# Kernel tuning notes

Hardware: AMD Instinct MI355X
Metric: run time of the kernel (lower is better)

Reference implementation:

```python
import jax, jax.numpy as jnp
import numpy as np

T, OBS, H, NOBJ = 32768, 256, 512, 4


def _xavier(key, shape):
    fan_in, fan_out = shape[0], shape[1]
    lim = jnp.sqrt(6.0 / (fan_in + fan_out)).astype(jnp.float32)
    return jax.random.uniform(key, shape, jnp.float32, -lim, lim)


def setup_inputs() -> dict:
    key = jax.random.key(0)
    ks = jax.random.split(key, 16)
    # weights stored as [in, out] so y = x @ W (same math as nn.Linear with W.T)
    return {
        "x": jax.random.normal(ks[0], (T, OBS), jnp.float32),
        "W_in0": _xavier(ks[1], (OBS, H)),
        "W_B0": _xavier(ks[2], (OBS, H)),
        "W_C0": _xavier(ks[3], (OBS, H)),
        "W_d0": _xavier(ks[4], (OBS, H)),
        "A_log0": jax.random.normal(ks[5], (H,), jnp.float32),
        "W_in1": _xavier(ks[6], (H, H)),
        "W_B1": _xavier(ks[7], (H, H)),
        "W_C1": _xavier(ks[8], (H, H)),
        "W_d1": _xavier(ks[9], (H, H)),
        "A_log1": jax.random.normal(ks[10], (H,), jnp.float32),
        "W_out": _xavier(ks[11], (H, NOBJ)),
        "b_out": jnp.zeros((NOBJ,), jnp.float32),
        "W_skip": _xavier(ks[12], (OBS, NOBJ)),
    }


def _mamba_layer(x, W_in, W_B, W_C, W_d, A_log):
    # x: [T, D_in] -> [T, H]
    x_state = x @ W_in           # [T, H]
    B = x @ W_B                  # [T, H]
    C = x @ W_C                  # [T, H]
    delta = jax.nn.sigmoid(x @ W_d)  # [T, H]
    A = -jnp.exp(A_log)          # [H]
    A_bar = jnp.exp(delta * A)   # [T, H], in (0, 1)
    Bx = B * x_state             # [T, H]

    def step(h, inp):
        a_t, bx_t = inp
        h = a_t * h + bx_t
        return h, h

    h0 = jnp.zeros((x_state.shape[-1],), x_state.dtype)
    _, h_seq = jax.lax.scan(step, h0, (A_bar, Bx))  # [T, H]
    return C * h_seq


def reference(x, W_in0, W_B0, W_C0, W_d0, A_log0,
              W_in1, W_B1, W_C1, W_d1, A_log1,
              W_out, b_out, W_skip):
    skip = x
    y = _mamba_layer(x, W_in0, W_B0, W_C0, W_d0, A_log0)
    y = _mamba_layer(y, W_in1, W_B1, W_C1, W_d1, A_log1)
    out = y @ W_out + b_out + skip @ W_skip  # [T, NOBJ]
    return out
```

## Files before the change

kernel.cpp:

```cpp
#include <hip/hip_runtime.h>

typedef __attribute__((ext_vector_type(8))) short short8;
typedef __attribute__((ext_vector_type(4))) float floatx4;

#define T_SIZE 32768
#define OBS    256
#define H      512
#define NC     1024
#define CHUNK  32
#define NGRP   64
#define GCH    16
#define SLAB   ((size_t)T_SIZE * 32)

__device__ __forceinline__ unsigned short f2bf(float f){
    union { float f; unsigned u; } v; v.f = f;
    unsigned u = v.u;
    u += 0x7FFFu + ((u >> 16) & 1u);
    return (unsigned short)(u >> 16);
}
__device__ __forceinline__ float bf2f(unsigned short u){
    union { unsigned u; float f; } v; v.u = ((unsigned)u) << 16; return v.f;
}

#define GLOAD_LDS16(g, l) \
    __builtin_amdgcn_global_load_lds((const __attribute__((address_space(1))) unsigned*)(g), \
                                     (__attribute__((address_space(3))) unsigned*)(l), 16, 0, 0)

__global__ void cast_x_kernel(const float* __restrict__ x, unsigned short* __restrict__ xb, int n4){
    int i = blockIdx.x * 256 + threadIdx.x;
    if (i < n4){
        float4 v = ((const float4*)x)[i];
        ushort4 o;
        o.x = f2bf(v.x); o.y = f2bf(v.y); o.z = f2bf(v.z); o.w = f2bf(v.w);
        ((ushort4*)xb)[i] = o;
    }
}

__global__ void tcast4_kernel(const float* __restrict__ W0, const float* __restrict__ W1,
                              const float* __restrict__ W2, const float* __restrict__ W3,
                              unsigned short* __restrict__ dst, int K, int KH){
    int idx = blockIdx.x * 256 + threadIdx.x;
    if (idx >= 4 * KH) return;
    int s   = idx / KH;
    int rem = idx - s * KH;
    int k = rem >> 9;
    int h = rem & 511;
    const float* W = (s == 0) ? W0 : (s == 1) ? W1 : (s == 2) ? W2 : W3;
    int b = h >> 4, hh = h & 15;
    dst[(size_t)((b * 4 + s) * 16 + hh) * K + k] = f2bf(W[(size_t)k * H + h]);
}

template<int K>
__global__ __launch_bounds__(256) void gemm_layer_kernel(
    const unsigned short* __restrict__ xb,
    const unsigned short* __restrict__ wt,
    const float* __restrict__ A_log,
    unsigned short* __restrict__ gT, unsigned short* __restrict__ bxT, unsigned short* __restrict__ CT,
    float* __restrict__ Pbuf, float* __restrict__ Hbuf)
{
    __shared__ unsigned short SM[2][8192];

    const int tid  = threadIdx.x;
    const int wave = tid >> 6;
    const int lane = tid & 63;
    const int ml   = lane & 15;
    const int quad = lane >> 4;
    const int wm   = wave & 1;
    const int wn   = wave >> 1;

    const int flat = blockIdx.y * 16 + blockIdx.x;
    const int xcd  = flat & 7;
    const int j    = flat >> 3;
    const int nb   = j & 15;
    const int mb   = (j >> 4) * 8 + xcd;
    const int m0   = mb * 128;

    const int srow = tid >> 2;
    const int sel  = (((tid & 3) ^ ((tid >> 3) & 3))) * 8;
    const int swz  = (ml >> 1) & 3;

    const unsigned short* pa0 = xb + (size_t)(m0 + srow) * K + sel;
    const unsigned short* pa1 = pa0 + (size_t)64 * K;
    const unsigned short* pb0 = wt + (size_t)(nb * 128 + srow) * K + sel;
    const unsigned short* pb1 = pb0 + (size_t)64 * K;

    const int ldsA0 = (wave * 64 + 0  ) * 8;
    const int ldsA1 = (wave * 64 + 256) * 8;

    const int rbaseA = (wm * 64 + ml) * 32 + (quad ^ swz) * 8;
    const int rbaseB = (wn * 64 + ml) * 32 + (quad ^ swz) * 8;

    floatx4 acc[4][4];
    #pragma unroll
    for (int i = 0; i < 4; i++)
        #pragma unroll
        for (int jj = 0; jj < 4; jj++)
            acc[i][jj] = (floatx4)(0.0f);

    constexpr int NK = K >> 5;
    GLOAD_LDS16(pa0, &SM[0][ldsA0]);
    GLOAD_LDS16(pa1, &SM[0][ldsA1]);
    GLOAD_LDS16(pb0, &SM[0][4096 + ldsA0]);
    GLOAD_LDS16(pb1, &SM[0][4096 + ldsA1]);

    #pragma unroll
    for (int kk = 0; kk < NK; ++kk){
        __syncthreads();
        constexpr_if_helper:;
        const int cur = kk & 1;
        if (kk + 1 < NK){
            const int nxt = cur ^ 1;
            const int ko  = (kk + 1) * 32;
            GLOAD_LDS16(pa0 + ko, &SM[nxt][ldsA0]);
            GLOAD_LDS16(pa1 + ko, &SM[nxt][ldsA1]);
            GLOAD_LDS16(pb0 + ko, &SM[nxt][4096 + ldsA0]);
            GLOAD_LDS16(pb1 + ko, &SM[nxt][4096 + ldsA1]);
        }

        short8 av[4], bv[4];
        #pragma unroll
        for (int i = 0; i < 4; i++)
            av[i] = *(const short8*)(&SM[cur][0] + rbaseA + i * 16 * 32);
        #pragma unroll
        for (int jj = 0; jj < 4; jj++)
            bv[jj] = *(const short8*)(&SM[cur][4096] + rbaseB + jj * 16 * 32);

        #pragma unroll
        for (int i = 0; i < 4; i++)
            #pragma unroll
            for (int jj = 0; jj < 4; jj++)
                acc[i][jj] = __builtin_amdgcn_mfma_f32_16x16x32_bf16(av[i], bv[jj], acc[i][jj], 0, 0, 0);
    }
    __syncthreads();

    unsigned short* SMe = &SM[0][0];
    float2* segbuf = (float2*)(SMe + 12288);
    const int col = wn * 16 + ml;
    const int h   = nb * 32 + col;
    const float Aneg = -expf(A_log[h]);

    #pragma unroll
    for (int i = 0; i < 4; i++){
        float p = 1.0f, hh = 0.0f;
        #pragma unroll
        for (int r = 0; r < 4; r++){
            int trow = wm * 64 + i * 16 + quad * 4 + r;
            float dv = acc[i][3][r];
            float delta = 1.0f / (1.0f + expf(-dv));
            unsigned short gb = f2bf(delta * Aneg);
            float a = expf(bf2f(gb));
            unsigned short bb = f2bf(acc[i][1][r] * acc[i][0][r]);
            SMe[        trow * 32 + col] = gb;
            SMe[4096 +  trow * 32 + col] = bb;
            SMe[8192 +  trow * 32 + col] = f2bf(acc[i][2][r]);
            hh = fmaf(a, hh, bf2f(bb));
            p *= a;
        }
        const int ch = wm * 2 + (i >> 1);
        const int s  = (i & 1) * 4 + quad;
        segbuf[(ch * 8 + s) * 32 + col] = make_float2(p, hh);
    }
    __syncthreads();
    {
        const short8* s8 = (const short8*)SMe;
        short8* dg = (short8*)(gT  + (size_t)nb * SLAB + (size_t)m0 * 32);
        short8* db = (short8*)(bxT + (size_t)nb * SLAB + (size_t)m0 * 32);
        short8* dc = (short8*)(CT  + (size_t)nb * SLAB + (size_t)m0 * 32);
        dg[tid] = s8[tid];        dg[tid + 256] = s8[tid + 256];
        db[tid] = s8[512 + tid];  db[tid + 256] = s8[768 + tid];
        dc[tid] = s8[1024 + tid]; dc[tid + 256] = s8[1280 + tid];
    }
    if (tid < 128){
        const int ccol = tid & 31, ch = tid >> 5;
        float P = 1.0f, Hc = 0.0f;
        #pragma unroll
        for (int s = 0; s < 8; s++){
            float2 ph = segbuf[(ch * 8 + s) * 32 + ccol];
            Hc = fmaf(ph.x, Hc, ph.y);
            P *= ph.x;
        }
        const int c = mb * 4 + ch;
        Pbuf[(size_t)c * H + nb * 32 + ccol] = P;
        Hbuf[(size_t)c * H + nb * 32 + ccol] = Hc;
    }
}

__global__ void scan2a_kernel(const float* __restrict__ P, const float* __restrict__ Hc,
                              float* __restrict__ Pg, float* __restrict__ Hg){
    const int g  = blockIdx.x;
    const int j4 = threadIdx.x * 4;
    float4 pc = {1.f,1.f,1.f,1.f}, hc = {0.f,0.f,0.f,0.f};
    #pragma unroll
    for (int i = 0; i < GCH; i++){
        size_t o = (size_t)(g * GCH + i) * H + j4;
        float4 P4 = *(const float4*)(P + o);
        float4 H4 = *(const float4*)(Hc + o);
        hc.x = fmaf(P4.x, hc.x, H4.x); pc.x *= P4.x;
        hc.y = fmaf(P4.y, hc.y, H4.y); pc.y *= P4.y;
        hc.z = fmaf(P4.z, hc.z, H4.z); pc.z *= P4.z;
        hc.w = fmaf(P4.w, hc.w, H4.w); pc.w *= P4.w;
    }
    *(float4*)(Pg + (size_t)g * H + j4) = pc;
    *(float4*)(Hg + (size_t)g * H + j4) = hc;
}

__global__ void scan2b_kernel(const float* __restrict__ Pg, const float* __restrict__ Hg,
                              float* __restrict__ Cg){
    const int j = threadIdx.x;
    float carry = 0.0f;
    for (int g0 = 0; g0 < NGRP; g0 += 8){
        float p[8], h[8];
        #pragma unroll
        for (int i = 0; i < 8; i++){
            p[i] = Pg[(size_t)(g0 + i) * H + j];
            h[i] = Hg[(size_t)(g0 + i) * H + j];
        }
        #pragma unroll
        for (int i = 0; i < 8; i++){
            Cg[(size_t)(g0 + i) * H + j] = carry;
            carry = fmaf(p[i], carry, h[i]);
        }
    }
}

__global__ void scan3_kernel(const unsigned short* __restrict__ gT, const unsigned short* __restrict__ bxT,
                             const unsigned short* __restrict__ CT,
                             const float* __restrict__ P, const float* __restrict__ Hc,
                             const float* __restrict__ Cg,
                             unsigned short* __restrict__ yb){
    int idx = blockIdx.x * 256 + threadIdx.x;
    int j4 = (idx & 127) * 4;
    int c  = idx >> 7;
    int nb = j4 >> 5, jj = j4 & 31;
    int grp = c >> 4;
    float4 h = *(const float4*)(Cg + (size_t)grp * H + j4);
    for (int cc = grp << 4; cc < c; ++cc){
        float4 P4 = *(const float4*)(P + (size_t)cc * H + j4);
        float4 H4 = *(const float4*)(Hc + (size_t)cc * H + j4);
        h.x = fmaf(P4.x, h.x, H4.x);
        h.y = fmaf(P4.y, h.y, H4.y);
        h.z = fmaf(P4.z, h.z, H4.z);
        h.w = fmaf(P4.w, h.w, H4.w);
    }
    size_t off = (size_t)nb * SLAB + (size_t)c * CHUNK * 32 + jj;
    size_t yo  = (size_t)c * CHUNK * H + j4;
    #pragma unroll 8
    for (int i = 0; i < CHUNK; i++){
        ushort4 gv = *(const ushort4*)(gT + off);
        ushort4 bv = *(const ushort4*)(bxT + off);
        ushort4 cv = *(const ushort4*)(CT + off);
        h.x = fmaf(expf(bf2f(gv.x)), h.x, bf2f(bv.x));
        h.y = fmaf(expf(bf2f(gv.y)), h.y, bf2f(bv.y));
        h.z = fmaf(expf(bf2f(gv.z)), h.z, bf2f(bv.z));
        h.w = fmaf(expf(bf2f(gv.w)), h.w, bf2f(bv.w));
        ushort4 o;
        o.x = f2bf(bf2f(cv.x) * h.x);
        o.y = f2bf(bf2f(cv.y) * h.y);
        o.z = f2bf(bf2f(cv.z) * h.z);
        o.w = f2bf(bf2f(cv.w) * h.w);
        *(ushort4*)(yb + yo) = o;
        off += 32; yo += H;
    }
}

__global__ __launch_bounds__(256) void final_kernel(const unsigned short* __restrict__ y2,
                                                    const unsigned short* __restrict__ xb,
                                                    const float* __restrict__ Wout,
                                                    const float* __restrict__ bout,
                                                    const float* __restrict__ Wskip,
                                                    float* __restrict__ out){
    int wave = threadIdx.x >> 6;
    int lane = threadIdx.x & 63;
    int t = blockIdx.x * 4 + wave;
    float s0 = 0.f, s1 = 0.f, s2 = 0.f, s3 = 0.f;
    const float4* W4 = (const float4*)Wout;
    #pragma unroll
    for (int k = lane; k < H; k += 64){
        float yv = bf2f(y2[(size_t)t * H + k]);
        float4 w = W4[k];
        s0 = fmaf(yv, w.x, s0); s1 = fmaf(yv, w.y, s1);
        s2 = fmaf(yv, w.z, s2); s3 = fmaf(yv, w.w, s3);
    }
    const float4* S4 = (const float4*)Wskip;
    #pragma unroll
    for (int k = lane; k < OBS; k += 64){
        float xv = bf2f(xb[(size_t)t * OBS + k]);
        float4 w = S4[k];
        s0 = fmaf(xv, w.x, s0); s1 = fmaf(xv, w.y, s1);
        s2 = fmaf(xv, w.z, s2); s3 = fmaf(xv, w.w, s3);
    }
    #pragma unroll
    for (int off = 32; off > 0; off >>= 1){
        s0 += __shfl_down(s0, off);
        s1 += __shfl_down(s1, off);
        s2 += __shfl_down(s2, off);
        s3 += __shfl_down(s3, off);
    }
    if (lane == 0){
        out[(size_t)t * 4 + 0] = s0 + bout[0];
        out[(size_t)t * 4 + 1] = s1 + bout[1];
        out[(size_t)t * 4 + 2] = s2 + bout[2];
        out[(size_t)t * 4 + 3] = s3 + bout[3];
    }
}

extern "C" void kernel_launch(void* const* d_in, const int* in_sizes, int n_in,
                              void* d_out, int out_size, void* d_ws, size_t ws_size,
                              hipStream_t stream)
{
    const float* x     = (const float*)d_in[0];
    const float* W_in0 = (const float*)d_in[1];
    const float* W_B0  = (const float*)d_in[2];
    const float* W_C0  = (const float*)d_in[3];
    const float* W_d0  = (const float*)d_in[4];
    const float* A0    = (const float*)d_in[5];
    const float* W_in1 = (const float*)d_in[6];
    const float* W_B1  = (const float*)d_in[7];
    const float* W_C1  = (const float*)d_in[8];
    const float* W_d1  = (const float*)d_in[9];
    const float* A1    = (const float*)d_in[10];
    const float* Wout  = (const float*)d_in[11];
    const float* bout  = (const float*)d_in[12];
    const float* Wskip = (const float*)d_in[13];
    float* out = (float*)d_out;

    char* ws = (char*)d_ws;
    size_t off = 0;
    auto alloc = [&](size_t bytes) -> void* {
        void* p = ws + off;
        off += (bytes + 255) & ~(size_t)255;
        return p;
    };
    unsigned short* xb  = (unsigned short*)alloc((size_t)T_SIZE * OBS * 2);
    unsigned short* yb  = (unsigned short*)alloc((size_t)T_SIZE * H * 2);
    unsigned short* Wt0 = (unsigned short*)alloc((size_t)4 * H * OBS * 2);
    unsigned short* Wt1 = (unsigned short*)alloc((size_t)4 * H * H * 2);
    unsigned short* gT  = (unsigned short*)alloc((size_t)T_SIZE * H * 2);
    unsigned short* bxT = (unsigned short*)alloc((size_t)T_SIZE * H * 2);
    unsigned short* CT  = (unsigned short*)alloc((size_t)T_SIZE * H * 2);
    float* Pbuf = (float*)alloc((size_t)NC * H * 4);
    float* Hbuf = (float*)alloc((size_t)NC * H * 4);
    float* Pg   = (float*)alloc((size_t)NGRP * H * 4);
    float* Hg   = (float*)alloc((size_t)NGRP * H * 4);
    float* Cg   = (float*)alloc((size_t)NGRP * H * 4);
    (void)ws_size; (void)in_sizes; (void)n_in; (void)out_size;

    cast_x_kernel<<<(T_SIZE * OBS / 4 + 255) / 256, 256, 0, stream>>>(x, xb, T_SIZE * OBS / 4);
    tcast4_kernel<<<(4 * OBS * H + 255) / 256, 256, 0, stream>>>(W_in0, W_B0, W_C0, W_d0, Wt0, OBS, OBS * H);
    tcast4_kernel<<<(4 * H   * H + 255) / 256, 256, 0, stream>>>(W_in1, W_B1, W_C1, W_d1, Wt1, H,   H * H);

    dim3 ggrid(16, 256);
    const int sgrid = NC * 128 / 256;

    gemm_layer_kernel<OBS><<<ggrid, 256, 0, stream>>>(xb, Wt0, A0, gT, bxT, CT, Pbuf, Hbuf);
    scan2a_kernel<<<NGRP, 128, 0, stream>>>(Pbuf, Hbuf, Pg, Hg);
    scan2b_kernel<<<1, H, 0, stream>>>(Pg, Hg, Cg);
    scan3_kernel<<<sgrid, 256, 0, stream>>>(gT, bxT, CT, Pbuf, Hbuf, Cg, yb);

    gemm_layer_kernel<H><<<ggrid, 256, 0, stream>>>(yb, Wt1, A1, gT, bxT, CT, Pbuf, Hbuf);
    scan2a_kernel<<<NGRP, 128, 0, stream>>>(Pbuf, Hbuf, Pg, Hg);
    scan2b_kernel<<<1, H, 0, stream>>>(Pg, Hg, Cg);
    scan3_kernel<<<sgrid, 256, 0, stream>>>(gT, bxT, CT, Pbuf, Hbuf, Cg, yb );

    final_kernel<<<T_SIZE / 4, 256, 0, stream>>>(yb, xb, Wout, bout, Wskip, out);
}
```

Measured before the change: 343.1 us.

## Deepen GEMM LDS pipeline to four stages with explicit vmcnt waits

Replaces the double-buffered LDS K-loop in the layer GEMM with a four-slot ring that prefetches three tiles ahead. It uses explicit s_waitcnt vmcnt counts and raw barriers instead of __syncthreads, so loads of later tiles stay in flight while the current tile is consumed. It also raises wave priority around the MFMA block. LDS use per block doubles to 64KB, which may reduce occupancy, and the hand-counted vmcnt values depend on GLOAD_LDS16 issuing exactly one counted load each.

```diff
diff --git a/kernel.cpp b/kernel.cpp
--- a/kernel.cpp
+++ b/kernel.cpp
@@ -58,7 +58,7 @@
     unsigned short* __restrict__ gT, unsigned short* __restrict__ bxT, unsigned short* __restrict__ CT,
     float* __restrict__ Pbuf, float* __restrict__ Hbuf)
 {
-    __shared__ unsigned short SM[2][8192];
+    __shared__ unsigned short SM[4][8192];
 
     const int tid  = threadIdx.x;
     const int wave = tid >> 6;
@@ -98,23 +98,30 @@
             acc[i][jj] = (floatx4)(0.0f);
 
     constexpr int NK = K >> 5;
-    GLOAD_LDS16(pa0, &SM[0][ldsA0]);
-    GLOAD_LDS16(pa1, &SM[0][ldsA1]);
-    GLOAD_LDS16(pb0, &SM[0][4096 + ldsA0]);
-    GLOAD_LDS16(pb1, &SM[0][4096 + ldsA1]);
+
+    #pragma unroll
+    for (int p = 0; p < 3; ++p){
+        const int ko = p * 32;
+        GLOAD_LDS16(pa0 + ko, &SM[p][ldsA0]);
+        GLOAD_LDS16(pa1 + ko, &SM[p][ldsA1]);
+        GLOAD_LDS16(pb0 + ko, &SM[p][4096 + ldsA0]);
+        GLOAD_LDS16(pb1 + ko, &SM[p][4096 + ldsA1]);
+    }
+    asm volatile("s_waitcnt vmcnt(8)" ::: "memory");
+    __builtin_amdgcn_s_barrier();
+    __builtin_amdgcn_sched_barrier(0);
 
     #pragma unroll
     for (int kk = 0; kk < NK; ++kk){
-        __syncthreads();
-        constexpr_if_helper:;
-        const int cur = kk & 1;
-        if (kk + 1 < NK){
-            const int nxt = cur ^ 1;
-            const int ko  = (kk + 1) * 32;
-            GLOAD_LDS16(pa0 + ko, &SM[nxt][ldsA0]);
-            GLOAD_LDS16(pa1 + ko, &SM[nxt][ldsA1]);
-            GLOAD_LDS16(pb0 + ko, &SM[nxt][4096 + ldsA0]);
-            GLOAD_LDS16(pb1 + ko, &SM[nxt][4096 + ldsA1]);
+        const int cur = kk & 3;
+
+        if (kk + 3 < NK){
+            const int ko  = (kk + 3) * 32;
+            const int nb4 = (kk + 3) & 3;
+            GLOAD_LDS16(pa0 + ko, &SM[nb4][ldsA0]);
+            GLOAD_LDS16(pa1 + ko, &SM[nb4][ldsA1]);
+            GLOAD_LDS16(pb0 + ko, &SM[nb4][4096 + ldsA0]);
+            GLOAD_LDS16(pb1 + ko, &SM[nb4][4096 + ldsA1]);
         }
 
         short8 av[4], bv[4];
@@ -125,11 +132,23 @@
         for (int jj = 0; jj < 4; jj++)
             bv[jj] = *(const short8*)(&SM[cur][4096] + rbaseB + jj * 16 * 32);
 
+        __builtin_amdgcn_s_setprio(1);
         #pragma unroll
         for (int i = 0; i < 4; i++)
             #pragma unroll
             for (int jj = 0; jj < 4; jj++)
                 acc[i][jj] = __builtin_amdgcn_mfma_f32_16x16x32_bf16(av[i], bv[jj], acc[i][jj], 0, 0, 0);
+        __builtin_amdgcn_s_setprio(0);
+
+        if (kk + 1 < NK){
+            const int hi = (kk + 3 < NK) ? (kk + 3) : (NK - 1);
+            const int vm = 4 * (hi - (kk + 1));
+            if (vm >= 8)      asm volatile("s_waitcnt vmcnt(8)" ::: "memory");
+            else if (vm == 4) asm volatile("s_waitcnt vmcnt(4)" ::: "memory");
+            else              asm volatile("s_waitcnt vmcnt(0)" ::: "memory");
+            __builtin_amdgcn_s_barrier();
+            __builtin_amdgcn_sched_barrier(0);
+        }
     }
     __syncthreads();
 
```

After: 334.2 us. -2.6%, faster.
